# Performance work log

Measured on AMD Instinct MI355X. Metric: run time of the kernel, lower is better.

## Reference

```python
import jax, jax.numpy as jnp
import numpy as np
import math

D_MODEL = 1024
N_HEADS = 16
D_K = D_MODEL // N_HEADS
MAX_LEN = 200
B, S = 64, 200


def _temporal_bias():
    # bias[i, j] = -0.1 * |i - j| / max_len, same for every head
    idx = jnp.arange(MAX_LEN, dtype=jnp.float32)
    dist = jnp.abs(idx[:, None] - idx[None, :])  # [L, L]
    tb = (-0.1 * dist / MAX_LEN)[None, None, :, :]  # [1, 1, L, L]
    return jnp.broadcast_to(tb, (1, N_HEADS, MAX_LEN, MAX_LEN))


def setup_inputs() -> dict:
    key = jax.random.key(0)
    ks = jax.random.split(key, 9)
    lim = 1.0 / math.sqrt(D_MODEL)
    def lin_w(k):
        return jax.random.uniform(k, (D_MODEL, D_MODEL), jnp.float32, -lim, lim)
    def lin_b(k):
        return jax.random.uniform(k, (D_MODEL,), jnp.float32, -lim, lim)
    return {
        "x": jax.random.normal(ks[0], (B, S, D_MODEL), jnp.float32),
        "mask": jnp.ones((B, 1, S, S), jnp.int32),
        "wq": lin_w(ks[1]), "bq": lin_b(ks[2]),
        "wk": lin_w(ks[3]), "bk": lin_b(ks[4]),
        "wv": lin_w(ks[5]), "bv": lin_b(ks[6]),
        "wo": lin_w(ks[7]), "bo": lin_b(ks[8]),
        "temporal_bias": _temporal_bias(),
    }


def reference(x, mask, wq, bq, wk, bk, wv, bv, wo, bo, temporal_bias):
    b, s, d = x.shape
    h, dk = N_HEADS, D_K
    scale = math.sqrt(dk)
    # torch Linear: y = x @ W.T + b; heads: [b, s, h, dk] -> [b, h, s, dk]
    q = (jnp.einsum('bsd,ed->bse', x, wq) + bq).reshape(b, s, h, dk).transpose(0, 2, 1, 3)
    k = (jnp.einsum('bsd,ed->bse', x, wk) + bk).reshape(b, s, h, dk).transpose(0, 2, 1, 3)
    v = (jnp.einsum('bsd,ed->bse', x, wv) + bv).reshape(b, s, h, dk).transpose(0, 2, 1, 3)
    scores = jnp.einsum('bhqd,bhkd->bhqk', q, k) / scale  # [b, h, s, s]
    scores = scores + temporal_bias[:, :, :s, :s]
    scores = jnp.where(mask == 0, jnp.float32(-1e9), scores)
    attn = jax.nn.softmax(scores, axis=-1)  # dropout is identity in eval mode
    ctx = jnp.einsum('bhqk,bhkd->bhqd', attn, v)
    ctx = ctx.transpose(0, 2, 1, 3).reshape(b, s, d)
    out = jnp.einsum('bsd,ed->bse', ctx, wo) + bo
    return out, attn
```

## Files before the change

### kernel.cpp

```cpp
#include <hip/hip_runtime.h>
#include <stdint.h>

typedef unsigned short u16;
typedef unsigned long long u64;
typedef __bf16 bf16x8 __attribute__((ext_vector_type(8)));
typedef float f32x4 __attribute__((ext_vector_type(4)));

#define MFMA16(a, b, c) __builtin_amdgcn_mfma_f32_16x16x32_bf16((a), (b), (c), 0, 0, 0)

#define BB 64
#define SS 200
#define DM 1024
#define NH 16
#define MM (BB * SS)
#define OUT0_ELEMS (MM * DM)

__device__ static inline u16 f2bf(float f) {
    __bf16 h = (__bf16)f;
    return __builtin_bit_cast(u16, h);
}

__device__ static inline bf16x8 load8(const u16* p) {
    uint4 u = *(const uint4*)p;
    union { uint4 u; bf16x8 b; } cv; cv.u = u; return cv.b;
}

__device__ static inline bf16x8 bzero8() {
    union { uint4 u; bf16x8 b; } cv; cv.u = make_uint4(0u, 0u, 0u, 0u); return cv.b;
}

__device__ static inline void gload_lds16(const void* g, void* l) {
    __builtin_amdgcn_global_load_lds(
        (const __attribute__((address_space(1))) void*)g,
        (__attribute__((address_space(3))) void*)l, 16, 0, 0);
}

__global__ __launch_bounds__(256) void convert_k(
    const float* __restrict__ x,
    const float* __restrict__ wq, const float* __restrict__ wk,
    const float* __restrict__ wv, const float* __restrict__ wo,
    u16* __restrict__ xb,
    u16* __restrict__ wqb, u16* __restrict__ wkb,
    u16* __restrict__ wvb, u16* __restrict__ wob)
{
    size_t i4 = (size_t)blockIdx.x * 256 + threadIdx.x;
    size_t e = i4 * 4;
    const float* src; u16* dst; size_t off;
    if (e < (size_t)OUT0_ELEMS) { src = x; dst = xb; off = e; }
    else {
        size_t we = e - OUT0_ELEMS;
        size_t w = we >> 20;
        off = we & 1048575u;
        src = (w == 0) ? wq : (w == 1) ? wk : (w == 2) ? wv : wo;
        dst = (w == 0) ? wqb : (w == 1) ? wkb : (w == 2) ? wvb : wob;
    }
    float4 v = *(const float4*)(src + off);
    union { u16 s[4]; uint2 u; } o;
    o.s[0] = f2bf(v.x); o.s[1] = f2bf(v.y); o.s[2] = f2bf(v.z); o.s[3] = f2bf(v.w);
    *(uint2*)(dst + off) = o.u;
}

__global__ __launch_bounds__(256) void maskbits_k(
    const int* __restrict__ mask, u64* __restrict__ bits)
{
    __shared__ unsigned char nb[4][64];
    const int wave = threadIdx.x >> 6, lane = threadIdx.x & 63;
    const int row = blockIdx.x * 4 + wave;
    const int* mp = mask + (size_t)row * 200;
    unsigned nib;
    if (lane < 50) {
        int4 v = *(const int4*)(mp + lane * 4);
        nib = (v.x ? 1u : 0u) | (v.y ? 2u : 0u) | (v.z ? 4u : 0u) | (v.w ? 8u : 0u);
    } else nib = 0xFu;
    nb[wave][lane] = (unsigned char)nib;
    __builtin_amdgcn_s_waitcnt(0);
    if (lane < 4) {
        const unsigned char* p = &nb[wave][lane * 16];
        u64 m = 0;
#pragma unroll
        for (int i = 0; i < 16; i++) m |= (u64)(p[i] & 0xFu) << (4 * i);
        bits[(size_t)row * 4 + lane] = m;
    }
}

template <int MODE>
__global__ __launch_bounds__(256) void gemm_k(
    const u16* __restrict__ A, const u16* __restrict__ W,
    const float* __restrict__ b0, const float* __restrict__ b1, const float* __restrict__ b2,
    u16* __restrict__ qo, u16* __restrict__ ko, u16* __restrict__ vto,
    float* __restrict__ outf)
{
    __shared__ __align__(16) u16 sm[8192];
    u16* As = sm;
    u16* Bs = sm + 4096;

    const int tid  = threadIdx.x;
    const int wave = tid >> 6;
    const int lane = tid & 63;
    const int quad = lane >> 4;
    const int l15  = lane & 15;
    const int n0   = blockIdx.x * 128;
    const int m0   = blockIdx.y * 128;
    const int seg  = (MODE == 0) ? (n0 >> 10) : 0;
    const int nn0  = n0 & 1023;
    const float* bias = (MODE == 1) ? b0 : (seg == 0 ? b0 : (seg == 1 ? b1 : b2));

    const int srow = wave * 16 + (lane >> 2);
    const int sk8  = (lane & 3) * 8;
    const int wuni = __builtin_amdgcn_readfirstlane(wave);

    f32x4 acc[4][4];
#pragma unroll
    for (int i = 0; i < 4; i++)
#pragma unroll
        for (int j = 0; j < 4; j++) acc[i][j] = (f32x4){0.f, 0.f, 0.f, 0.f};

    const int wr = (wave >> 1) * 64;
    const int wc = (wave & 1) * 64;

    const u16* Ag = A + (size_t)m0 * 1024;
    const u16* Wg = W + (size_t)n0 * 1024;

    for (int kc = 0; kc < 1024; kc += 32) {
        __syncthreads();
#pragma unroll
        for (int r = 0; r < 2; r++) {
            int row = r * 64 + srow;
            gload_lds16(Ag + (size_t)row * 1024 + kc + sk8, &As[(r * 64 + wuni * 16) * 32]);
        }
#pragma unroll
        for (int r = 0; r < 2; r++) {
            int row = r * 64 + srow;
            gload_lds16(Wg + (size_t)row * 1024 + kc + sk8, &Bs[(r * 64 + wuni * 16) * 32]);
        }
        __syncthreads();

        bf16x8 af[4], bf[4];
#pragma unroll
        for (int mt = 0; mt < 4; mt++) af[mt] = load8(&As[(wr + mt * 16 + l15) * 32 + quad * 8]);
#pragma unroll
        for (int nt = 0; nt < 4; nt++) bf[nt] = load8(&Bs[(wc + nt * 16 + l15) * 32 + quad * 8]);
#pragma unroll
        for (int mt = 0; mt < 4; mt++)
#pragma unroll
            for (int nt = 0; nt < 4; nt++)
                acc[mt][nt] = MFMA16(af[mt], bf[nt], acc[mt][nt]);
    }

    if (MODE == 1) {
#pragma unroll
        for (int nt = 0; nt < 4; nt++) {
            int n = n0 + wc + nt * 16 + l15;
            float bv = bias[n];
#pragma unroll
            for (int mt = 0; mt < 4; mt++)
#pragma unroll
                for (int r = 0; r < 4; r++) {
                    int m = m0 + wr + mt * 16 + quad * 4 + r;
                    __builtin_nontemporal_store(acc[mt][nt][r] + bv,
                                                &outf[(size_t)m * 1024 + n]);
                }
        }
    } else if (seg == 2) {
#pragma unroll
        for (int nt = 0; nt < 4; nt++) {
            int nn = nn0 + wc + nt * 16 + l15;
            float bv = bias[nn];
            int hh = nn >> 6, d = nn & 63;
#pragma unroll
            for (int mt = 0; mt < 4; mt++) {
                int mbase = m0 + wr + mt * 16 + quad * 4;
                int b = mbase / 200, s = mbase - b * 200;
                union { u16 q[4]; uint2 u; } pk;
#pragma unroll
                for (int r = 0; r < 4; r++) pk.q[r] = f2bf(acc[mt][nt][r] + bv);
                *(uint2*)&vto[((size_t)(b * 16 + hh) * 64 + d) * 200 + s] = pk.u;
            }
        }
    } else {
        u16* dst = (seg == 0) ? qo : ko;
        float bv[4];
#pragma unroll
        for (int nt = 0; nt < 4; nt++) bv[nt] = bias[nn0 + wc + nt * 16 + l15];
#pragma unroll
        for (int h2 = 0; h2 < 2; h2++) {
            __syncthreads();
            if ((wave >> 1) == h2) {
#pragma unroll
                for (int nt = 0; nt < 4; nt++)
#pragma unroll
                    for (int mt = 0; mt < 4; mt++)
#pragma unroll
                        for (int r = 0; r < 4; r++) {
                            int rl = mt * 16 + quad * 4 + r;
                            int c  = wc + nt * 16 + l15;
                            sm[rl * 128 + (c ^ ((rl & 7) << 4))] = f2bf(acc[mt][nt][r] + bv[nt]);
                        }
            }
            __syncthreads();
#pragma unroll
            for (int j = 0; j < 4; j++) {
                int idx = tid + j * 256;
                int rl = idx >> 4, c8 = (idx & 15) * 8;
                int c8s = c8 ^ ((rl & 7) << 4);
                uint4 vv = *(const uint4*)&sm[rl * 128 + c8s];
                *(uint4*)&dst[((size_t)(m0 + h2 * 64 + rl)) * 1024 + nn0 + c8] = vv;
            }
        }
    }
}

__global__ __launch_bounds__(256, 4) void attn_k(
    const u16* __restrict__ qg, const u16* __restrict__ kg, const u16* __restrict__ vtg,
    const u64* __restrict__ mbits,
    float* __restrict__ attn_out, u16* __restrict__ ctxb)
{
    __shared__ __align__(16) u16 Pb[4][16 * 208];

    const int tid  = threadIdx.x;
    const int wave = tid >> 6;
    const int lane = tid & 63;
    const int quad = lane >> 4;
    const int l15  = lane & 15;

    const int task = blockIdx.x * 4 + wave;
    const int bh   = task / 13;
    const int i0   = (task - bh * 13) * 16;
    const int b    = bh >> 4;
    const int h    = bh & 15;

    u16* pb = Pb[wave];

    const u16* qkbase = qg + (size_t)b * 200 * 1024 + h * 64;
    int qi = i0 + l15;
    const u16* qrow = qkbase + (size_t)(qi < 200 ? qi : 0) * 1024;
    bf16x8 aq0, aq1;
    if (qi < 200) { aq0 = load8(qrow + quad * 8); aq1 = load8(qrow + 32 + quad * 8); }
    else          { aq0 = bzero8(); aq1 = bzero8(); }

    const int ib = i0 + quad * 4;
    const u16* kbase = kg + (size_t)b * 200 * 1024 + h * 64;
    const u64* mrow = mbits + (size_t)b * 200 * 4;
    const float TBC = -0.1f / 200.0f;

    f32x4 sv[13];
    f32x4 mxr = (f32x4){-3.0e38f, -3.0e38f, -3.0e38f, -3.0e38f};
    u64 mw[4];

#pragma unroll
    for (int t = 0; t < 13; t++) {
        int kj = t * 16 + l15;
        const u16* krow = kbase + (size_t)(kj < 200 ? kj : 0) * 1024;
        bf16x8 bk0, bk1;
        if (kj < 200) { bk0 = load8(krow + quad * 8); bk1 = load8(krow + 32 + quad * 8); }
        else          { bk0 = bzero8(); bk1 = bzero8(); }
        f32x4 z = (f32x4){0.f, 0.f, 0.f, 0.f};
        z = MFMA16(aq0, bk0, z);
        z = MFMA16(aq1, bk1, z);

        if ((t & 3) == 0) {
            const int c = t >> 2;
#pragma unroll
            for (int r = 0; r < 4; r++) {
                int ia = ib + r;
                mw[r] = mrow[(size_t)(ia < 200 ? ia : 0) * 4 + c];
            }
        }
        const int col = t * 16 + l15;
        const int sh  = (t & 3) * 16 + l15;
        const float fc = (float)col;
        f32x4 s;
#pragma unroll
        for (int r = 0; r < 4; r++) {
            int ia = ib + r;
            float val = z[r] * 0.125f + TBC * fabsf((float)ia - fc);
            if (!((mw[r] >> sh) & 1)) val = -1e9f;
            s[r] = (ia < 200 && col < 200) ? val : -3.0e38f;
            mxr[r] = fmaxf(mxr[r], s[r]);
        }
        sv[t] = s;
    }

#pragma unroll
    for (int m = 1; m < 16; m <<= 1)
#pragma unroll
        for (int r = 0; r < 4; r++)
            mxr[r] = fmaxf(mxr[r], __shfl_xor(mxr[r], m, 64));

    f32x4 sum = (f32x4){0.f, 0.f, 0.f, 0.f};
#pragma unroll
    for (int t = 0; t < 13; t++) {
        f32x4 s = sv[t];
#pragma unroll
        for (int r = 0; r < 4; r++) { s[r] = __expf(s[r] - mxr[r]); sum[r] += s[r]; }
        sv[t] = s;
    }
#pragma unroll
    for (int m = 1; m < 16; m <<= 1)
#pragma unroll
        for (int r = 0; r < 4; r++)
            sum[r] += __shfl_xor(sum[r], m, 64);

    f32x4 inv;
#pragma unroll
    for (int r = 0; r < 4; r++) inv[r] = (sum[r] > 0.f) ? 1.f / sum[r] : 0.f;

    float* aop = attn_out + (size_t)bh * 40000;
#pragma unroll
    for (int t = 0; t < 13; t++) {
        const int col = t * 16 + l15;
#pragma unroll
        for (int r = 0; r < 4; r++) {
            int ia = ib + r;
            float a = sv[t][r] * inv[r];
            pb[(quad * 4 + r) * 208 + col] = (col < 200) ? f2bf(a) : (u16)0;
            if (ia < 200 && col < 200)
                __builtin_nontemporal_store(a, aop + (size_t)ia * 200 + col);
        }
    }

    f32x4 ctx[4];
#pragma unroll
    for (int nt = 0; nt < 4; nt++) ctx[nt] = (f32x4){0.f, 0.f, 0.f, 0.f};
    const u16* vb = vtg + (size_t)bh * 64 * 200;
#pragma unroll
    for (int kc = 0; kc < 224; kc += 32) {
        int j0 = kc + quad * 8;
        bf16x8 af = (j0 < 208) ? load8(pb + l15 * 208 + j0) : bzero8();
#pragma unroll
        for (int nt = 0; nt < 4; nt++) {
            bf16x8 bvf = (j0 < 200) ? load8(vb + (nt * 16 + l15) * 200 + j0) : bzero8();
            ctx[nt] = MFMA16(af, bvf, ctx[nt]);
        }
    }

#pragma unroll
    for (int nt = 0; nt < 4; nt++)
#pragma unroll
        for (int r = 0; r < 4; r++)
            pb[(quad * 4 + r) * 208 + nt * 16 + l15] = f2bf(ctx[nt][r]);

#pragma unroll
    for (int k = 0; k < 2; k++) {
        int rr = k * 8 + (lane >> 3), ss = lane & 7;
        int ia = i0 + rr;
        uint4 val = *(const uint4*)&pb[rr * 208 + ss * 8];
        if (ia < 200)
            *(uint4*)&ctxb[((size_t)b * 200 + ia) * 1024 + h * 64 + ss * 8] = val;
    }
}

extern "C" void kernel_launch(void* const* d_in, const int* in_sizes, int n_in,
                              void* d_out, int out_size, void* d_ws, size_t ws_size,
                              hipStream_t stream) {
    const float* x    = (const float*)d_in[0];
    const int*   mask = (const int*)d_in[1];
    const float* wq   = (const float*)d_in[2];
    const float* bq   = (const float*)d_in[3];
    const float* wk   = (const float*)d_in[4];
    const float* bk   = (const float*)d_in[5];
    const float* wv   = (const float*)d_in[6];
    const float* bv   = (const float*)d_in[7];
    const float* wo   = (const float*)d_in[8];
    const float* bo   = (const float*)d_in[9];

    float* out  = (float*)d_out;
    float* attn = out + OUT0_ELEMS;

    char* ws = (char*)d_ws;
    u16* xb    = (u16*)(ws);
    u16* wqb   = (u16*)(ws + 26214400);
    u16* wkb   = (u16*)(ws + 28311552);
    u16* wvb   = (u16*)(ws + 30408704);
    u16* wob   = (u16*)(ws + 32505856);
    u16* qb    = (u16*)(ws + 34603008);
    u16* kb    = (u16*)(ws + 60817408);
    u16* vtb   = (u16*)(ws + 87031808);
    u16* ctxb  = (u16*)(ws + 113246208);
    u64* mbits = (u64*)(ws + 139460608);

    convert_k<<<dim3(16896), dim3(256), 0, stream>>>(x, wq, wk, wv, wo, xb, wqb, wkb, wvb, wob);

    maskbits_k<<<dim3(3200), dim3(256), 0, stream>>>(mask, mbits);

    gemm_k<0><<<dim3(24, 100), dim3(256), 0, stream>>>(
        xb, wqb, bq, bk, bv, qb, kb, vtb, nullptr);

    attn_k<<<dim3(3328), dim3(256), 0, stream>>>(qb, kb, vtb, mbits, attn, ctxb);

    gemm_k<1><<<dim3(8, 100), dim3(256), 0, stream>>>(
        ctxb, wob, bo, nullptr, nullptr, nullptr, nullptr, nullptr, out);
}
```

Before: 565.2 us.

## Software-pipeline K, mask and V loads in attention kernel with register prefetch

Attention kernel now prefetches K tiles four steps ahead and mask words one chunk ahead in the QK^T loop. It also double-buffers V and P fragments in the PV loop, with the first V load issued before the attn-probability store phase. Occupancy hints move from launch_bounds min-blocks to waves_per_eu(3,4). The aim is to hide global load latency behind MFMA and softmax work, at the cost of more live registers that could reduce occupancy or cause spills.

Measured after the change: 533.6 us. 1.06x faster.

```diff
diff --git a/kernel.cpp b/kernel.cpp
--- a/kernel.cpp
+++ b/kernel.cpp
@@ -210,7 +210,8 @@
     }
 }
 
-__global__ __launch_bounds__(256, 4) void attn_k(
+__global__ __launch_bounds__(256) __attribute__((amdgpu_waves_per_eu(3, 4)))
+void attn_k(
     const u16* __restrict__ qg, const u16* __restrict__ kg, const u16* __restrict__ vtg,
     const u64* __restrict__ mbits,
     float* __restrict__ attn_out, u16* __restrict__ ctxb)
@@ -243,29 +244,40 @@
     const u64* mrow = mbits + (size_t)b * 200 * 4;
     const float TBC = -0.1f / 200.0f;
 
+#define KLOAD(T, A, B) do {                                              \
+        int kj_ = (T) * 16 + l15;                                        \
+        const u16* kr_ = kbase + (size_t)(kj_ < 200 ? kj_ : 0) * 1024;   \
+        if (kj_ < 200) { (A) = load8(kr_ + quad * 8);                    \
+                         (B) = load8(kr_ + 32 + quad * 8); }             \
+        else           { (A) = bzero8(); (B) = bzero8(); }               \
+    } while (0)
+
+#define MLD(R, C) mrow[(size_t)((ib + (R)) < 200 ? (ib + (R)) : 0) * 4 + (C)]
+#define LOADM(C, D) do { D[0] = MLD(0, C); D[1] = MLD(1, C);             \
+                         D[2] = MLD(2, C); D[3] = MLD(3, C); } while (0)
+
+    bf16x8 ka[4], kb4[4];
+    KLOAD(0, ka[0], kb4[0]);
+    KLOAD(1, ka[1], kb4[1]);
+    KLOAD(2, ka[2], kb4[2]);
+    KLOAD(3, ka[3], kb4[3]);
+
+    u64 mwc[4], mwn[4];
+    LOADM(0, mwc);
+
     f32x4 sv[13];
     f32x4 mxr = (f32x4){-3.0e38f, -3.0e38f, -3.0e38f, -3.0e38f};
-    u64 mw[4];
 
 #pragma unroll
     for (int t = 0; t < 13; t++) {
-        int kj = t * 16 + l15;
-        const u16* krow = kbase + (size_t)(kj < 200 ? kj : 0) * 1024;
-        bf16x8 bk0, bk1;
-        if (kj < 200) { bk0 = load8(krow + quad * 8); bk1 = load8(krow + 32 + quad * 8); }
-        else          { bk0 = bzero8(); bk1 = bzero8(); }
+        bf16x8 b0 = ka[t & 3], b1 = kb4[t & 3];
+        if (t + 4 < 13) KLOAD(t + 4, ka[t & 3], kb4[t & 3]);
+        if ((t & 3) == 0 && (t >> 2) < 3) LOADM((t >> 2) + 1, mwn);
+
         f32x4 z = (f32x4){0.f, 0.f, 0.f, 0.f};
-        z = MFMA16(aq0, bk0, z);
-        z = MFMA16(aq1, bk1, z);
-
-        if ((t & 3) == 0) {
-            const int c = t >> 2;
-#pragma unroll
-            for (int r = 0; r < 4; r++) {
-                int ia = ib + r;
-                mw[r] = mrow[(size_t)(ia < 200 ? ia : 0) * 4 + c];
-            }
-        }
+        z = MFMA16(aq0, b0, z);
+        z = MFMA16(aq1, b1, z);
+
         const int col = t * 16 + l15;
         const int sh  = (t & 3) * 16 + l15;
         const float fc = (float)col;
@@ -274,11 +286,14 @@
         for (int r = 0; r < 4; r++) {
             int ia = ib + r;
             float val = z[r] * 0.125f + TBC * fabsf((float)ia - fc);
-            if (!((mw[r] >> sh) & 1)) val = -1e9f;
+            if (!((mwc[r] >> sh) & 1)) val = -1e9f;
             s[r] = (ia < 200 && col < 200) ? val : -3.0e38f;
             mxr[r] = fmaxf(mxr[r], s[r]);
         }
         sv[t] = s;
+
+        if ((t & 3) == 3) { mwc[0] = mwn[0]; mwc[1] = mwn[1];
+                            mwc[2] = mwn[2]; mwc[3] = mwn[3]; }
     }
 
 #pragma unroll
@@ -304,6 +319,26 @@
     f32x4 inv;
 #pragma unroll
     for (int r = 0; r < 4; r++) inv[r] = (sum[r] > 0.f) ? 1.f / sum[r] : 0.f;
+
+    const u16* vb = vtg + (size_t)bh * 64 * 200;
+    bf16x8 vf[2][4], afr[2];
+
+#define VLOADF(KC7, BUF) do {                                            \
+        int j0v_ = (KC7) * 32 + quad * 8;                                \
+        if (j0v_ < 200) {                                                \
+            vf[BUF][0] = load8(vb + (0 * 16 + l15) * 200 + j0v_);        \
+            vf[BUF][1] = load8(vb + (1 * 16 + l15) * 200 + j0v_);        \
+            vf[BUF][2] = load8(vb + (2 * 16 + l15) * 200 + j0v_);        \
+            vf[BUF][3] = load8(vb + (3 * 16 + l15) * 200 + j0v_);        \
+        } else { vf[BUF][0] = bzero8(); vf[BUF][1] = bzero8();           \
+                 vf[BUF][2] = bzero8(); vf[BUF][3] = bzero8(); }         \
+    } while (0)
+#define AFLOAD(KC7, BUF) do {                                            \
+        int j0a_ = (KC7) * 32 + quad * 8;                                \
+        afr[BUF] = (j0a_ < 208) ? load8(pb + l15 * 208 + j0a_) : bzero8(); \
+    } while (0)
+
+    VLOADF(0, 0);
 
     float* aop = attn_out + (size_t)bh * 40000;
 #pragma unroll
@@ -319,19 +354,19 @@
         }
     }
 
+    AFLOAD(0, 0);
+
     f32x4 ctx[4];
 #pragma unroll
     for (int nt = 0; nt < 4; nt++) ctx[nt] = (f32x4){0.f, 0.f, 0.f, 0.f};
-    const u16* vb = vtg + (size_t)bh * 64 * 200;
-#pragma unroll
-    for (int kc = 0; kc < 224; kc += 32) {
-        int j0 = kc + quad * 8;
-        bf16x8 af = (j0 < 208) ? load8(pb + l15 * 208 + j0) : bzero8();
-#pragma unroll
-        for (int nt = 0; nt < 4; nt++) {
-            bf16x8 bvf = (j0 < 200) ? load8(vb + (nt * 16 + l15) * 200 + j0) : bzero8();
-            ctx[nt] = MFMA16(af, bvf, ctx[nt]);
-        }
+
+#pragma unroll
+    for (int k7 = 0; k7 < 7; k7++) {
+        if (k7 < 6) { VLOADF(k7 + 1, (k7 + 1) & 1); AFLOAD(k7 + 1, (k7 + 1) & 1); }
+        ctx[0] = MFMA16(afr[k7 & 1], vf[k7 & 1][0], ctx[0]);
+        ctx[1] = MFMA16(afr[k7 & 1], vf[k7 & 1][1], ctx[1]);
+        ctx[2] = MFMA16(afr[k7 & 1], vf[k7 & 1][2], ctx[2]);
+        ctx[3] = MFMA16(afr[k7 & 1], vf[k7 & 1][3], ctx[3]);
     }
 
 #pragma unroll
```
